# Optimization experiments

Measured on AMD Instinct MI355X. Metric: run time of the kernel, lower is better.

The kernel has to match this reference:

```python
import jax, jax.numpy as jnp
import numpy as np

INF = 1.0e12
V, EMB, H, H2 = 50000, 300, 512, 1024
EDGE, EEMB = 4, 32
B, TS, TQ = 16, 400, 33
MAX_OOV = 100
EXT = V + MAX_OOV
COV_HYPER = 1.0


def gru_cell(x, h, Wi, Wh, bi, bh):
    # torch GRU cell, gate order r,z,n
    gx = x @ Wi.T + bi
    gh = h @ Wh.T + bh
    hd = h.shape[-1]
    r = jax.nn.sigmoid(gx[:, :hd] + gh[:, :hd])
    z = jax.nn.sigmoid(gx[:, hd:2 * hd] + gh[:, hd:2 * hd])
    n = jnp.tanh(gx[:, 2 * hd:] + r * gh[:, 2 * hd:])
    return (1.0 - z) * n + z * h


def gru_scan(xs, h0, Wi, Wh, bi, bh, reverse=False):
    def step(h, x):
        hn = gru_cell(x, h, Wi, Wh, bi, bh)
        return hn, hn
    return jax.lax.scan(step, h0, xs, reverse=reverse)


def setup_inputs() -> dict:
    key = jax.random.key(0)
    ks = iter(jax.random.split(key, 64))
    def rp(*shape):
        return jax.random.normal(next(ks), shape, jnp.float32) * 0.05
    d = {}
    d['enc_emb'] = rp(V, EMB); d['ans_emb'] = rp(EDGE, EEMB); d['dec_emb'] = rp(V, EMB)
    in0 = EMB + EEMB
    d['eWi0'] = rp(2, 3 * H, in0); d['eWh0'] = rp(2, 3 * H, H); d['ebi0'] = rp(2, 3 * H); d['ebh0'] = rp(2, 3 * H)
    d['eWi1'] = rp(2, 3 * H, 2 * H); d['eWh1'] = rp(2, 3 * H, H); d['ebi1'] = rp(2, 3 * H); d['ebh1'] = rp(2, 3 * H)
    d['trans_W'] = rp(H2, H2); d['trans_b'] = rp(H2)
    d['upd_W'] = rp(H2, 2 * H2); d['gate_W'] = rp(H2, 2 * H2)
    din0 = EMB + H2
    d['dWi0'] = rp(3 * H2, din0); d['dWh0'] = rp(3 * H2, H2); d['dbi0'] = rp(3 * H2); d['dbh0'] = rp(3 * H2)
    d['dWi1'] = rp(3 * H2, H2); d['dWh1'] = rp(3 * H2, H2); d['dbi1'] = rp(3 * H2); d['dbh1'] = rp(3 * H2)
    d['dtrans_W'] = rp(H2, H2); d['dtrans_b'] = rp(H2)
    d['pW1'] = rp(H2, 2 * H2); d['pb1'] = rp(H2); d['pW2'] = rp(V, H2); d['pb2'] = rp(V)
    d['input_s'] = jax.random.randint(next(ks), (B, TS), 1, V)
    ext = jax.random.randint(next(ks), (B, TS), 0, EXT)
    d['ext_src_ids'] = ext.at[0, 0].set(EXT - 1)  # pin num_oov = MAX_OOV
    d['input_q'] = jax.random.randint(next(ks), (B, TQ), 1, V)
    d['input_a'] = jax.random.randint(next(ks), (B, TS), 0, EDGE)
    d['s_pos'] = jax.random.randint(next(ks), (B, TS), 0, TS)
    return d


def reference(enc_emb, ans_emb, dec_emb,
              eWi0, eWh0, ebi0, ebh0, eWi1, eWh1, ebi1, ebh1,
              trans_W, trans_b, upd_W, gate_W,
              dWi0, dWh0, dbi0, dbh0, dWi1, dWh1, dbi1, dbh1,
              dtrans_W, dtrans_b, pW1, pb1, pW2, pb2,
              input_s, ext_src_ids, input_q, input_a, s_pos):
    mask = jnp.sign(input_s)  # [B,TS] (all ones by construction)
    # ---------------- encoder ----------------
    emb = jnp.concatenate([enc_emb[input_s], ans_emb[input_a]], -1)  # [B,TS,EMB+EEMB]
    xs = emb.transpose(1, 0, 2)  # [TS,B,*]
    h0 = jnp.zeros((B, H), emb.dtype)
    h_list = []
    for (Wi, Wh, bi, bh) in ((eWi0, eWh0, ebi0, ebh0), (eWi1, eWh1, ebi1, ebh1)):
        hf, yf = gru_scan(xs, h0, Wi[0], Wh[0], bi[0], bh[0])
        hb, yb = gru_scan(xs, h0, Wi[1], Wh[1], bi[1], bh[1], reverse=True)
        xs = jnp.concatenate([yf, yb], -1)
        h_list.append(jnp.concatenate([hf, hb], -1))  # [B,H2]
    output = xs.transpose(1, 0, 2)  # [B,TS,H2]
    memories = output @ trans_W.T + trans_b
    # gated self-attention
    energies = jnp.einsum('btd,bsd->bts', output, memories)
    energies = jnp.where(mask[:, None, :] == 0, -INF, energies)
    scores = jax.nn.softmax(energies, -1)
    ctx = jnp.einsum('bts,bsd->btd', scores, output)
    inp = jnp.concatenate([output, ctx], -1)
    f_t = jnp.tanh(inp @ upd_W.T)
    g_t = jax.nn.sigmoid(inp @ gate_W.T)
    self_out = g_t * f_t + (1.0 - g_t) * output
    # answer-sentence attention (on memories, per original code)
    ans = jnp.where(input_a[..., None] == 0, 1.0, memories)
    e = memories * ans
    e = jnp.where(mask[..., None] == 0, -INF, e)
    e = jax.nn.softmax(e, axis=1)
    enc_out = self_out + e * memories
    # ---------------- decoder ----------------
    mem_d = enc_out @ dtrans_W.T + dtrans_b  # [B,TS,H2]
    emb_q = dec_emb[input_q[:, :-1]].transpose(1, 0, 2)  # [Tt,B,EMB]
    b_idx = jnp.arange(B)[:, None]

    def step(carry, emb_t):
        h0c, h1c, ctx_c, cov = carry
        rnn_in = jnp.concatenate([emb_t, ctx_c], -1)
        h0n = gru_cell(rnn_in, h0c, dWi0, dWh0, dbi0, dbh0)
        h1n = gru_cell(h0n, h1c, dWi1, dWh1, dbi1, dbh1)
        energy = jnp.einsum('bd,btd->bt', h1n, mem_d)
        sen_e = jnp.where(mask == 0, -INF, energy)
        cov_e = sen_e * (1.0 - cov)
        attn = jax.nn.softmax(cov_e, -1)
        new_ctx = jnp.einsum('bt,btd->bd', attn, mem_d)
        cov_loss = jnp.sum(jnp.minimum(attn, cov)) / B * COV_HYPER
        new_cov = cov + attn
        hid = jnp.tanh(jnp.concatenate([h1n, new_ctx], -1) @ pW1.T + pb1)
        logits = hid @ pW2.T + pb2
        ext = jnp.concatenate([logits, jnp.zeros((B, MAX_OOV), logits.dtype)], -1)
        out = jnp.full((B, EXT), -INF, logits.dtype).at[b_idx, ext_src_ids].max(cov_e)
        out = jnp.where(out == -INF, 0.0, out)
        lg = ext + out
        lg = jnp.where(lg == 0.0, -INF, lg)
        return (h0n, h1n, new_ctx, new_cov), (lg, cov_loss)

    init = (h_list[0], h_list[1], jnp.zeros((B, H2), emb.dtype), jnp.zeros((B, TS), emb.dtype))
    _, (lgs, covl) = jax.lax.scan(step, init, emb_q)
    return lgs.transpose(1, 0, 2), jnp.sum(covl) / lgs.shape[0]


if __name__ == '__main__':
    o = reference(**setup_inputs())
    print(o[0].shape, o[1])
```

## Files before the change

### kernel.cpp

```cpp
#include <hip/hip_runtime.h>
#include <stdint.h>

#define TSN 400
#define NB 16
#define HENC 512
#define HD2 1024
#define G3E 1536
#define G3D 3072
#define EMBD 300
#define AEMB 32
#define NV 50000
#define NEXT 50100
#define NVP 50176
#define NTT 32
#define NEG_INF (-1.0e12f)

typedef __attribute__((ext_vector_type(8))) short bf16x8;
typedef __attribute__((ext_vector_type(4))) float f32x4;

__device__ __forceinline__ ushort f2bf(float f) {
  unsigned u = __float_as_uint(f);
  unsigned r = (u + 0x7fffu + ((u >> 16) & 1u)) >> 16;
  return (ushort)r;
}
__device__ __forceinline__ float bf2f(ushort h) {
  return __uint_as_float((unsigned)h << 16);
}
__device__ __forceinline__ unsigned agat_ld(const unsigned* p) {
  return __hip_atomic_load(p, __ATOMIC_RELAXED, __HIP_MEMORY_SCOPE_AGENT);
}
__device__ __forceinline__ void agat_st(unsigned* p, unsigned v) {
  __hip_atomic_store(p, v, __ATOMIC_RELAXED, __HIP_MEMORY_SCOPE_AGENT);
}

__global__ __launch_bounds__(256) void k_embed_bf(
    const float* __restrict__ enc_emb, const float* __restrict__ ans_emb,
    const int* __restrict__ input_s, const int* __restrict__ input_a,
    ushort* __restrict__ X0)
{
  long i = (long)blockIdx.x*256 + threadIdx.x;
  if (i >= (long)TSN*NB*384) return;
  int c = (int)(i % 384);
  long r = i / 384;
  int b = (int)(r % NB);
  int t = (int)(r / NB);
  float v = 0.f;
  if (c < EMBD) v = enc_emb[(long)input_s[b*TSN + t]*EMBD + c];
  else if (c < 332) v = ans_emb[(long)input_a[b*TSN + t]*AEMB + (c - EMBD)];
  X0[i] = f2bf(v);
}

__global__ __launch_bounds__(256) void k_embq_bf(
    const float* __restrict__ dec_emb, const int* __restrict__ input_q,
    ushort* __restrict__ EQ)
{
  long i = (long)blockIdx.x*256 + threadIdx.x;
  if (i >= (long)NTT*NB*320) return;
  int c = (int)(i % 320);
  long r = i / 320;
  int b = (int)(r % NB);
  int s = (int)(r / NB);
  EQ[i] = (c < EMBD) ? f2bf(dec_emb[(long)input_q[b*33 + s]*EMBD + c]) : (ushort)0;
}

__global__ __launch_bounds__(256) void k_castw(
    const float* __restrict__ src, ushort* __restrict__ dst,
    int Nsrc, long total, int Ksrc, int Kdst, int ldsrc, int coloff)
{
  long i = (long)blockIdx.x*256 + threadIdx.x;
  if (i >= total) return;
  int k = (int)(i % Kdst);
  long n = i / Kdst;
  float v = (n < Nsrc && k < Ksrc) ? src[n*ldsrc + coloff + k] : 0.f;
  dst[i] = f2bf(v);
}

__global__ __launch_bounds__(256) void k_cast(
    const float* __restrict__ s, ushort* __restrict__ d, long n)
{
  long i = (long)blockIdx.x*256 + threadIdx.x;
  if (i >= n) return;
  d[i] = f2bf(s[i]);
}

__global__ __launch_bounds__(256) void k_transpose_hh(
    const ushort* __restrict__ in, ushort* __restrict__ out)
{
  __shared__ ushort tb[32][33];
  int b = blockIdx.z;
  int r0 = blockIdx.x*32, c0 = blockIdx.y*32;
  int tx = threadIdx.x & 31, ty = threadIdx.x >> 5;
  #pragma unroll
  for (int i = 0; i < 32; i += 8) {
    int r = r0 + ty + i, c = c0 + tx;
    tb[ty+i][tx] = (r < TSN) ? in[((long)b*TSN + r)*1024 + c] : (ushort)0;
  }
  __syncthreads();
  #pragma unroll
  for (int i = 0; i < 32; i += 8) {
    int c = c0 + ty + i, r = r0 + tx;
    out[((long)b*1024 + c)*448 + r] = tb[tx][ty+i];
  }
}

__global__ __launch_bounds__(256) void k_mfma_nt(
    const ushort* __restrict__ Ab, const ushort* __restrict__ Wb,
    const float* __restrict__ bias, float* __restrict__ Cb, ushort* __restrict__ C2b,
    int M, int N, int K, int lda, int ldw, int ldc,
    long sA, long sW, long sC, long sBias, int accum, int act)
{
  __shared__ ushort As[64][72];
  __shared__ ushort Ws[64][72];
  const ushort* A = Ab + (long)blockIdx.z * sA;
  const ushort* W = Wb + (long)blockIdx.z * sW;
  float* C = Cb ? Cb + (long)blockIdx.z * sC : nullptr;
  const float* bi = bias ? bias + (long)blockIdx.z * sBias : nullptr;
  const int m0 = blockIdx.x*64, n0 = blockIdx.y*64;
  const int tid = threadIdx.x;
  const int wave = tid >> 6, lane = tid & 63;
  const int wm = wave >> 1, wn = wave & 1;
  const int lr = lane & 15, kg = lane >> 4;
  f32x4 acc[2][2] = {};
  for (int k0 = 0; k0 < K; k0 += 64) {
    __syncthreads();
    #pragma unroll
    for (int it = 0; it < 2; ++it) {
      int sidx = tid + it*256;
      int r = sidx >> 3, c = (sidx & 7)*8;
      bf16x8 av = {};
      bf16x8 wv = {};
      if (m0 + r < M) av = *(const bf16x8*)&A[(long)(m0+r)*lda + k0 + c];
      if (n0 + r < N) wv = *(const bf16x8*)&W[(long)(n0+r)*ldw + k0 + c];
      *(bf16x8*)&As[r][c] = av;
      *(bf16x8*)&Ws[r][c] = wv;
    }
    __syncthreads();
    #pragma unroll
    for (int kk = 0; kk < 2; ++kk) {
      bf16x8 af[2], bf[2];
      #pragma unroll
      for (int mt = 0; mt < 2; ++mt)
        af[mt] = *(const bf16x8*)&As[wm*32 + mt*16 + lr][kk*32 + kg*8];
      #pragma unroll
      for (int nt = 0; nt < 2; ++nt)
        bf[nt] = *(const bf16x8*)&Ws[wn*32 + nt*16 + lr][kk*32 + kg*8];
      #pragma unroll
      for (int mt = 0; mt < 2; ++mt)
        #pragma unroll
        for (int nt = 0; nt < 2; ++nt)
          acc[mt][nt] = __builtin_amdgcn_mfma_f32_16x16x32_bf16(af[mt], bf[nt], acc[mt][nt], 0, 0, 0);
    }
  }
  #pragma unroll
  for (int mt = 0; mt < 2; ++mt) {
    #pragma unroll
    for (int r = 0; r < 4; ++r) {
      int m = m0 + wm*32 + mt*16 + kg*4 + r;
      if (m >= M) continue;
      #pragma unroll
      for (int nt = 0; nt < 2; ++nt) {
        int n = n0 + wn*32 + nt*16 + lr;
        if (n >= N) continue;
        float v = acc[mt][nt][r];
        if (accum && C) v += C[(long)m*ldc + n];
        if (bi)    v += bi[n];
        if (act == 1) v = tanhf(v);
        else if (act == 2) v = 1.f/(1.f + expf(-v));
        if (C) C[(long)m*ldc + n] = v;
        if (C2b) C2b[(long)blockIdx.z*sC + (long)m*ldc + n] = f2bf(v);
      }
    }
  }
}

__global__ __launch_bounds__(256, 1) void k_scan_mfma(
    const ushort* __restrict__ GXf, const ushort* __restrict__ GXb,
    const ushort* __restrict__ Whb,
    const float* __restrict__ bh,
    ushort* __restrict__ Ybf, int bmajor,
    float* __restrict__ hfin,
    ushort* __restrict__ hpp,
    int* __restrict__ slots)
{
  const int bid = blockIdx.x;
  const int tid = threadIdx.x;
  const int wg = bid*4 + (tid >> 6);
  const int lane = tid & 63;
  const int lr = lane & 15, kg = lane >> 4;
  const int dir = wg >> 5, jt = wg & 31;
  const int j = jt*16 + lr;
  __shared__ ushort hsm[16][520];
  const ushort* Wp0 = Whb + ((long)(dir*G3E + j)        << 9) + kg*8;
  const ushort* Wp1 = Whb + ((long)(dir*G3E + 512 + j)  << 9) + kg*8;
  const ushort* Wp2 = Whb + ((long)(dir*G3E + 1024 + j) << 9) + kg*8;
  bf16x8 W0[16], W1[16], W2[16];
  #pragma unroll
  for (int i = 0; i < 16; ++i) {
    W0[i] = *(const bf16x8*)(Wp0 + i*32);
    W1[i] = *(const bf16x8*)(Wp1 + i*32);
    W2[i] = *(const bf16x8*)(Wp2 + i*32);
  }
  const float bh0 = bh[dir*G3E + j];
  const float bh1 = bh[dir*G3E + 512 + j];
  const float bh2 = bh[dir*G3E + 1024 + j];
  const ushort* GX = dir ? GXb : GXf;
  unsigned* hppu = (unsigned*)hpp;
  int* myslot = slots + dir*256 + (bid & 7)*32;
  int* dslots = slots + dir*256;
  float hreg[4] = {0.f, 0.f, 0.f, 0.f};
  float g0[4], g1[4], g2[4];
  {
    const int t0 = dir ? (TSN - 1) : 0;
    const ushort* gxp = GX + (long)t0*NB*G3E + j;
    #pragma unroll
    for (int r = 0; r < 4; ++r) {
      const ushort* g = gxp + (long)(kg*4 + r)*G3E;
      g0[r] = bf2f(g[0]); g1[r] = bf2f(g[512]); g2[r] = bf2f(g[1024]);
    }
  }
  for (int s = 0; s < TSN; ++s) {
    const int cur = s & 1;
    {
      const unsigned* hin = hppu + (cur*2 + dir)*4096;
      unsigned vdw[16];
      #pragma unroll
      for (int i = 0; i < 16; ++i) vdw[i] = agat_ld(hin + i*256 + tid);
      #pragma unroll
      for (int i = 0; i < 16; ++i) {
        int idx = i*256 + tid;
        int b = idx >> 8, jd = idx & 255;
        *(unsigned*)&hsm[b][jd*2] = vdw[i];
      }
    }
    __syncthreads();
    f32x4 a0 = {}, a1 = {}, a2 = {};
    #pragma unroll
    for (int i = 0; i < 16; ++i) {
      bf16x8 hf = *(const bf16x8*)&hsm[lr][kg*8 + i*32];
      a0 = __builtin_amdgcn_mfma_f32_16x16x32_bf16(hf, W0[i], a0, 0, 0, 0);
      a1 = __builtin_amdgcn_mfma_f32_16x16x32_bf16(hf, W1[i], a1, 0, 0, 0);
      a2 = __builtin_amdgcn_mfma_f32_16x16x32_bf16(hf, W2[i], a2, 0, 0, 0);
    }
    const int t = dir ? (TSN - 1 - s) : s;
    const int obase = ((cur^1)*2 + dir)*16*512;
    float hsave[4];
    #pragma unroll
    for (int r = 0; r < 4; ++r) {
      int b = kg*4 + r;
      float rr = 1.f/(1.f + expf(-(g0[r] + a0[r] + bh0)));
      float zz = 1.f/(1.f + expf(-(g1[r] + a1[r] + bh1)));
      float nn = tanhf(g2[r] + rr*(a2[r] + bh2));
      float hn = (1.f - zz)*nn + zz*hreg[r];
      hreg[r] = hn;
      hsave[r] = hn;
      unsigned hv = f2bf(hn);
      unsigned pv = (unsigned)__shfl_xor((int)hv, 1);
      if ((lr & 1) == 0)
        agat_st(hppu + ((obase + b*512 + j) >> 1), hv | (pv << 16));
    }
    if (s + 1 < TSN) {
      asm volatile("s_waitcnt vmcnt(0)" ::: "memory");
      __syncthreads();
      if (tid == 0)
        agat_st((unsigned*)myslot, (unsigned)(s + 1));
      {
        const int tn = dir ? (TSN - 2 - s) : (s + 1);
        const ushort* gxp = GX + (long)tn*NB*G3E + j;
        #pragma unroll
        for (int r = 0; r < 4; ++r) {
          const ushort* g = gxp + (long)(kg*4 + r)*G3E;
          g0[r] = bf2f(g[0]); g1[r] = bf2f(g[512]); g2[r] = bf2f(g[1024]);
        }
      }
      #pragma unroll
      for (int r = 0; r < 4; ++r) {
        int b = kg*4 + r;
        long yi = bmajor ? ((long)b*TSN + t)*1024 + dir*512 + j
                         : ((long)t*NB + b)*1024 + dir*512 + j;
        Ybf[yi] = f2bf(hsave[r]);
      }
      if (tid < 8) {
        while ((int)agat_ld((const unsigned*)(dslots + tid*32)) < s + 1)
          __builtin_amdgcn_s_sleep(1);
      }
      __syncthreads();
    } else {
      #pragma unroll
      for (int r = 0; r < 4; ++r) {
        int b = kg*4 + r;
        long yi = bmajor ? ((long)b*TSN + t)*1024 + dir*512 + j
                         : ((long)t*NB + b)*1024 + dir*512 + j;
        Ybf[yi] = f2bf(hsave[r]);
        hfin[b*1024 + dir*512 + j] = hsave[r];
      }
    }
  }
}

__global__ __launch_bounds__(256) void k_softmax_bf(
    const float* __restrict__ E, ushort* __restrict__ S)
{
  long row = blockIdx.x;
  const float* x = E + row*TSN;
  ushort* o = S + row*448;
  int tid = threadIdx.x;
  float v0 = (tid < TSN) ? x[tid] : -INFINITY;
  float v1 = (tid + 256 < TSN) ? x[tid + 256] : -INFINITY;
  __shared__ float red[256];
  red[tid] = fmaxf(v0, v1); __syncthreads();
  for (int oo = 128; oo; oo >>= 1) { if (tid < oo) red[tid] = fmaxf(red[tid], red[tid+oo]); __syncthreads(); }
  float m = red[0]; __syncthreads();
  float e0 = (tid < TSN) ? expf(v0 - m) : 0.f;
  float e1 = (tid + 256 < TSN) ? expf(v1 - m) : 0.f;
  red[tid] = e0 + e1; __syncthreads();
  for (int oo = 128; oo; oo >>= 1) { if (tid < oo) red[tid] += red[tid+oo]; __syncthreads(); }
  float inv = 1.f/red[0];
  if (tid < 192) o[tid + 256] = (tid + 256 < TSN) ? f2bf(e1*inv) : (ushort)0;
  o[tid] = f2bf(e0*inv);
}

__global__ __launch_bounds__(256) void k_ansatt2(
    const ushort* __restrict__ memsb, const float* __restrict__ ft,
    const float* __restrict__ gt, const ushort* __restrict__ outpb,
    const int* __restrict__ input_a, ushort* __restrict__ encb)
{
  int b = blockIdx.x >> 2;
  int d = (blockIdx.x & 3)*256 + threadIdx.x;
  __shared__ int ia[TSN];
  for (int i = threadIdx.x; i < TSN; i += 256) ia[i] = input_a[b*TSN + i];
  __syncthreads();
  float m = -INFINITY;
  #pragma unroll 4
  for (int t = 0; t < TSN; ++t) {
    float v = bf2f(memsb[((long)b*TSN + t)*1024 + d]);
    float e = ia[t] ? v*v : v;
    m = fmaxf(m, e);
  }
  float ssum = 0.f;
  #pragma unroll 4
  for (int t = 0; t < TSN; ++t) {
    float v = bf2f(memsb[((long)b*TSN + t)*1024 + d]);
    float e = ia[t] ? v*v : v;
    ssum += expf(e - m);
  }
  float inv = 1.f/ssum;
  #pragma unroll 4
  for (int t = 0; t < TSN; ++t) {
    long idx = ((long)b*TSN + t)*1024 + d;
    float v = bf2f(memsb[idx]);
    float e = ia[t] ? v*v : v;
    float gg = gt[idx];
    float selfo = gg*ft[idx] + (1.f - gg)*bf2f(outpb[idx]);
    encb[idx] = f2bf(selfo + expf(e - m)*inv*v);
  }
}

__global__ __launch_bounds__(128) void k_gru_dec(
    const ushort* __restrict__ A1, const ushort* __restrict__ W1,
    const ushort* __restrict__ A2, const ushort* __restrict__ W2,
    const float* __restrict__ gxadd, const float* __restrict__ bi,
    const float* __restrict__ bh,
    const float* __restrict__ hprev, float* __restrict__ hout,
    ushort* __restrict__ houtb, ushort* __restrict__ catb)
{
  const int wv = threadIdx.x >> 6;
  const int lane = threadIdx.x & 63;
  const int lr = lane & 15, kg = lane >> 4;
  const int j = blockIdx.x*16 + lr;
  const int kb = wv*512;
  __shared__ float psum[6][16][16];
  const ushort* w1p0 = W1 + ((long)(j)        << 10) + kb + kg*8;
  const ushort* w1p1 = W1 + ((long)(1024 + j) << 10) + kb + kg*8;
  const ushort* w1p2 = W1 + ((long)(2048 + j) << 10) + kb + kg*8;
  const ushort* w2p0 = W2 + ((long)(j)        << 10) + kb + kg*8;
  const ushort* w2p1 = W2 + ((long)(1024 + j) << 10) + kb + kg*8;
  const ushort* w2p2 = W2 + ((long)(2048 + j) << 10) + kb + kg*8;
  const ushort* a1p = A1 + lr*1024 + kb + kg*8;
  const ushort* a2p = A2 + lr*1024 + kb + kg*8;
  f32x4 x0 = {}, x1 = {}, x2 = {}, h0 = {}, h1 = {}, h2 = {};
  #pragma unroll 4
  for (int k0 = 0; k0 < 512; k0 += 32) {
    bf16x8 a1v = *(const bf16x8*)(a1p + k0);
    bf16x8 a2v = *(const bf16x8*)(a2p + k0);
    x0 = __builtin_amdgcn_mfma_f32_16x16x32_bf16(a1v, *(const bf16x8*)(w1p0 + k0), x0, 0, 0, 0);
    x1 = __builtin_amdgcn_mfma_f32_16x16x32_bf16(a1v, *(const bf16x8*)(w1p1 + k0), x1, 0, 0, 0);
    x2 = __builtin_amdgcn_mfma_f32_16x16x32_bf16(a1v, *(const bf16x8*)(w1p2 + k0), x2, 0, 0, 0);
    h0 = __builtin_amdgcn_mfma_f32_16x16x32_bf16(a2v, *(const bf16x8*)(w2p0 + k0), h0, 0, 0, 0);
    h1 = __builtin_amdgcn_mfma_f32_16x16x32_bf16(a2v, *(const bf16x8*)(w2p1 + k0), h1, 0, 0, 0);
    h2 = __builtin_amdgcn_mfma_f32_16x16x32_bf16(a2v, *(const bf16x8*)(w2p2 + k0), h2, 0, 0, 0);
  }
  if (wv == 1) {
    #pragma unroll
    for (int r = 0; r < 4; ++r) {
      int b = kg*4 + r;
      psum[0][b][lr] = x0[r]; psum[1][b][lr] = x1[r]; psum[2][b][lr] = x2[r];
      psum[3][b][lr] = h0[r]; psum[4][b][lr] = h1[r]; psum[5][b][lr] = h2[r];
    }
  }
  __syncthreads();
  if (wv == 0) {
    float bi0 = bi ? bi[j] : 0.f, bi1 = bi ? bi[1024 + j] : 0.f, bi2 = bi ? bi[2048 + j] : 0.f;
    float bh0 = bh[j], bh1 = bh[1024 + j], bh2 = bh[2048 + j];
    #pragma unroll
    for (int r = 0; r < 4; ++r) {
      int b = kg*4 + r;
      float gxa0 = gxadd ? gxadd[(long)b*G3D + j]        : 0.f;
      float gxa1 = gxadd ? gxadd[(long)b*G3D + 1024 + j] : 0.f;
      float gxa2 = gxadd ? gxadd[(long)b*G3D + 2048 + j] : 0.f;
      float gx0 = x0[r] + psum[0][b][lr] + gxa0 + bi0;
      float gx1 = x1[r] + psum[1][b][lr] + gxa1 + bi1;
      float gx2 = x2[r] + psum[2][b][lr] + gxa2 + bi2;
      float gh0 = h0[r] + psum[3][b][lr] + bh0;
      float gh1 = h1[r] + psum[4][b][lr] + bh1;
      float gh2 = h2[r] + psum[5][b][lr] + bh2;
      float rr = 1.f/(1.f + expf(-(gx0 + gh0)));
      float zz = 1.f/(1.f + expf(-(gx1 + gh1)));
      float nn = tanhf(gx2 + rr*gh2);
      float hp = hprev[b*1024 + j];
      float hn = (1.f - zz)*nn + zz*hp;
      hout[b*1024 + j] = hn;
      houtb[b*1024 + j] = f2bf(hn);
      if (catb) catb[(long)b*2048 + j] = f2bf(hn);
    }
  }
}

__global__ __launch_bounds__(1024) void k_dec_attn2(
    const ushort* __restrict__ h1b, const ushort* __restrict__ memdb,
    float* __restrict__ cov, float* __restrict__ covOut, float* __restrict__ covacc,
    ushort* __restrict__ ctxn, ushort* __restrict__ catb)
{
  const int b = blockIdx.x, tid = threadIdx.x;
  const int wv = tid >> 6, ln = tid & 63;
  __shared__ float sc[TSN];
  __shared__ float at[TSN];
  __shared__ float red[1024];
  float hreg[16];
  {
    bf16x8 hv0 = *(const bf16x8*)&h1b[b*1024 + ln*16];
    bf16x8 hv1 = *(const bf16x8*)&h1b[b*1024 + ln*16 + 8];
    #pragma unroll
    for (int e = 0; e < 8; ++e) { hreg[e] = bf2f((ushort)hv0[e]); hreg[8+e] = bf2f((ushort)hv1[e]); }
  }
  for (int t = wv; t < TSN; t += 16) {
    const ushort* row = memdb + ((long)b*TSN + t)*1024 + ln*16;
    bf16x8 r0 = *(const bf16x8*)row;
    bf16x8 r1 = *(const bf16x8*)(row + 8);
    float p = 0.f;
    #pragma unroll
    for (int e = 0; e < 8; ++e) p += hreg[e]*bf2f((ushort)r0[e]) + hreg[8+e]*bf2f((ushort)r1[e]);
    #pragma unroll
    for (int off = 32; off; off >>= 1) p += __shfl_xor(p, off);
    if (ln == 0) sc[t] = p;
  }
  __syncthreads();
  float ce = -INFINITY, co = 0.f;
  if (tid < TSN) { co = cov[b*TSN + tid]; ce = sc[tid]*(1.f - co); }
  red[tid] = ce; __syncthreads();
  for (int o = 512; o; o >>= 1) { if (tid < o) red[tid] = fmaxf(red[tid], red[tid+o]); __syncthreads(); }
  float m = red[0]; __syncthreads();
  float ex = (tid < TSN) ? expf(ce - m) : 0.f;
  red[tid] = ex; __syncthreads();
  for (int o = 512; o; o >>= 1) { if (tid < o) red[tid] += red[tid+o]; __syncthreads(); }
  float inv = 1.f/red[0]; __syncthreads();
  float closs = 0.f;
  if (tid < TSN) {
    float a = ex*inv;
    at[tid] = a;
    cov[b*TSN + tid] = co + a;
    covOut[b*TSN + tid] = ce;
    closs = fminf(a, co);
  }
  red[tid] = closs; __syncthreads();
  for (int o = 512; o; o >>= 1) { if (tid < o) red[tid] += red[tid+o]; __syncthreads(); }
  if (tid == 0) atomicAdd(covacc, red[0]);
  __syncthreads();
  float s = 0.f;
  const ushort* col = memdb + (long)b*TSN*1024 + tid;
  #pragma unroll 8
  for (int t = 0; t < TSN; ++t) s += at[t]*bf2f(col[(long)t*1024]);
  ushort hv = f2bf(s);
  ctxn[b*1024 + tid] = hv;
  catb[(long)b*2048 + 1024 + tid] = hv;
}

__global__ __launch_bounds__(128) void k_hid(
    const ushort* __restrict__ catb, const ushort* __restrict__ W,
    const float* __restrict__ pb1, ushort* __restrict__ hidb)
{
  const int wv = threadIdx.x >> 6;
  const int lane = threadIdx.x & 63;
  const int lr = lane & 15, kg = lane >> 4;
  const int n = blockIdx.x*16 + lr;
  const int kb = wv*1024;
  __shared__ float ps[16][16];
  f32x4 acc = {};
  const ushort* ap = catb + lr*2048 + kb + kg*8;
  const ushort* wp = W + ((long)n << 11) + kb + kg*8;
  #pragma unroll 8
  for (int k0 = 0; k0 < 1024; k0 += 32)
    acc = __builtin_amdgcn_mfma_f32_16x16x32_bf16(*(const bf16x8*)(ap + k0), *(const bf16x8*)(wp + k0), acc, 0, 0, 0);
  if (wv == 1) {
    #pragma unroll
    for (int r = 0; r < 4; ++r) ps[kg*4 + r][lr] = acc[r];
  }
  __syncthreads();
  if (wv == 0) {
    float bv = pb1[n];
    #pragma unroll
    for (int r = 0; r < 4; ++r) {
      int b = kg*4 + r;
      hidb[b*1024 + n] = f2bf(tanhf(acc[r] + ps[b][lr] + bv));
    }
  }
}

__global__ __launch_bounds__(256) void k_logits_all(
    const ushort* __restrict__ hidAll,
    const ushort* __restrict__ pW2b,
    const float* __restrict__ pb2,
    float* __restrict__ outp)
{
  const int wave = threadIdx.x >> 6, lane = threadIdx.x & 63;
  const int lr = lane & 15, kg = lane >> 4;
  const int n0 = blockIdx.x*256 + wave*64;
  const int m0 = blockIdx.y*128;
  f32x4 acc[8][4] = {};
  for (int k0 = 0; k0 < 1024; k0 += 32) {
    bf16x8 bfr[4];
    #pragma unroll
    for (int nt = 0; nt < 4; ++nt)
      bfr[nt] = *(const bf16x8*)&pW2b[(long)(n0 + nt*16 + lr)*1024 + k0 + kg*8];
    #pragma unroll
    for (int mt = 0; mt < 8; ++mt) {
      bf16x8 af = *(const bf16x8*)&hidAll[(long)(m0 + mt*16 + lr)*1024 + k0 + kg*8];
      #pragma unroll
      for (int nt = 0; nt < 4; ++nt)
        acc[mt][nt] = __builtin_amdgcn_mfma_f32_16x16x32_bf16(af, bfr[nt], acc[mt][nt], 0, 0, 0);
    }
  }
  #pragma unroll
  for (int nt = 0; nt < 4; ++nt) {
    int v = n0 + nt*16 + lr;
    if (v >= NEXT) continue;
    float pb = (v < NV) ? pb2[v] : 0.f;
    #pragma unroll
    for (int mt = 0; mt < 8; ++mt) {
      #pragma unroll
      for (int r = 0; r < 4; ++r) {
        int m = m0 + mt*16 + kg*4 + r;
        int s = m >> 4, b = m & 15;
        float e = (v < NV) ? (acc[mt][nt][r] + pb) : 0.f;
        if (e == 0.f) e = NEG_INF;
        outp[((long)b*NTT + s)*NEXT + v] = e;
      }
    }
  }
}

__device__ __forceinline__ float dec_f(unsigned e) {
  return (e & 0x80000000u) ? __uint_as_float(e ^ 0x80000000u) : __uint_as_float(~e);
}
__global__ __launch_bounds__(512) void k_compose_all(
    const int* __restrict__ ids, const float* __restrict__ coveAll,
    unsigned* __restrict__ ubuf, float* __restrict__ outp)
{
  int b = blockIdx.x, tid = threadIdx.x;
  int v = 0;
  if (tid < TSN) v = ids[b*TSN + tid];
  unsigned* up = ubuf + (long)b*NEXT;
  for (int s = 0; s < NTT; ++s) {
    if (tid < TSN) {
      float ce = coveAll[((long)s*NB + b)*TSN + tid];
      unsigned bb = __float_as_uint(ce);
      unsigned enc = (bb & 0x80000000u) ? ~bb : (bb | 0x80000000u);
      atomicMax(&up[v], enc);
    }
    __syncthreads();
    if (tid < TSN) {
      unsigned u = __hip_atomic_load(&up[v], __ATOMIC_RELAXED, __HIP_MEMORY_SCOPE_AGENT);
      float o = dec_f(u);
      long oi = ((long)b*NTT + s)*NEXT + v;
      float e = outp[oi];
      if (e == NEG_INF) e = 0.f;
      float lg = e + o;
      if (lg == 0.f) lg = NEG_INF;
      outp[oi] = lg;
    }
    __syncthreads();
    if (tid < TSN)
      __hip_atomic_store(&up[v], 0u, __ATOMIC_RELAXED, __HIP_MEMORY_SCOPE_AGENT);
    __syncthreads();
  }
}

__global__ void k_covout(const float* __restrict__ covacc, float* __restrict__ outp)
{
  outp[(long)NB*NTT*NEXT] = covacc[0] * (1.0f/(NB*NTT));
}

extern "C" void kernel_launch(void* const* d_in, const int* in_sizes, int n_in,
                              void* d_out, int out_size, void* d_ws, size_t ws_size,
                              hipStream_t stream) {
  (void)in_sizes; (void)n_in; (void)out_size; (void)ws_size;
  const float* enc_emb = (const float*)d_in[0];
  const float* ans_emb = (const float*)d_in[1];
  const float* dec_emb = (const float*)d_in[2];
  const float* eWi0 = (const float*)d_in[3];
  const float* eWh0 = (const float*)d_in[4];
  const float* ebi0 = (const float*)d_in[5];
  const float* ebh0 = (const float*)d_in[6];
  const float* eWi1 = (const float*)d_in[7];
  const float* eWh1 = (const float*)d_in[8];
  const float* ebi1 = (const float*)d_in[9];
  const float* ebh1 = (const float*)d_in[10];
  const float* trans_W = (const float*)d_in[11];
  const float* trans_b = (const float*)d_in[12];
  const float* upd_W = (const float*)d_in[13];
  const float* gate_W = (const float*)d_in[14];
  const float* dWi0 = (const float*)d_in[15];
  const float* dWh0 = (const float*)d_in[16];
  const float* dbi0 = (const float*)d_in[17];
  const float* dbh0 = (const float*)d_in[18];
  const float* dWi1 = (const float*)d_in[19];
  const float* dWh1 = (const float*)d_in[20];
  const float* dbi1 = (const float*)d_in[21];
  const float* dbh1 = (const float*)d_in[22];
  const float* dtrans_W = (const float*)d_in[23];
  const float* dtrans_b = (const float*)d_in[24];
  const float* pW1 = (const float*)d_in[25];
  const float* pb1 = (const float*)d_in[26];
  const float* pW2 = (const float*)d_in[27];
  const float* pb2 = (const float*)d_in[28];
  const int* input_s = (const int*)d_in[29];
  const int* ext_ids = (const int*)d_in[30];
  const int* input_q = (const int*)d_in[31];
  const int* input_a = (const int*)d_in[32];
  float* out = (float*)d_out;

  float* ws = (float*)d_ws;
  size_t off = 0;
  auto alloc = [&](size_t n) { float* p = ws + off; off += (n + 15) & ~(size_t)15; return p; };
  auto alloch = [&](size_t nh) { return (ushort*)alloc((nh + 1) / 2); };

  ushort* hpp  = alloch(2ull*2*NB*HENC);
  int*   bar   = (int*)alloc(2048);
  float* covacc= alloc(4);
  float* cov   = alloc(NB*TSN);
  unsigned* ubuf = (unsigned*)alloc((size_t)NB*NEXT);
  float* hfin0 = alloc(NB*HD2);
  float* hfin1 = alloc(NB*HD2);
  float* dh0   = alloc(2ull*NB*HD2);
  float* dh1   = alloc(2ull*NB*HD2);
  ushort* h0b  = alloch(2ull*NB*HD2);
  ushort* h1b  = alloch(2ull*NB*HD2);
  ushort* ctxbf= alloch(2ull*NB*HD2);
  ushort* catbf= alloch((size_t)NB*2048);
  ushort* hidAll = alloch((size_t)NTT*NB*HD2);
  float* coveAll = alloc((size_t)NTT*NB*TSN);

  ushort* eWi0c   = alloch(2ull*G3E*384);
  ushort* eWi1c   = alloch(2ull*G3E*1024);
  ushort* Whb0    = alloch(2ull*G3E*HENC);
  ushort* Whb1    = alloch(2ull*G3E*HENC);
  ushort* transWb = alloch(1024ull*1024);
  ushort* updWb   = alloch(1024ull*2048);
  ushort* gateWb  = alloch(1024ull*2048);
  ushort* dtransWb= alloch(1024ull*1024);
  ushort* dWi0e   = alloch(3072ull*320);
  ushort* dWi0c   = alloch(3072ull*1024);
  ushort* dWh0b   = alloch(3072ull*1024);
  ushort* dWi1b   = alloch(3072ull*1024);
  ushort* dWh1b   = alloch(3072ull*1024);
  ushort* pW1b    = alloch(1024ull*2048);

  size_t regionStart = off;
  float*  GXr  = alloc(2ull*6400*G3E);
  ushort* GXbf = (ushort*)GXr;
  ushort* X0c  = alloch(6400ull*384);
  ushort* Y0bf = alloch(6400ull*1024);
  float*  ft   = alloc(6400ull*HD2);
  ushort* pW2b   = (ushort*)(ws + regionStart);
  ushort* outpTb = (ushort*)(ws + regionStart + 26000000);

  ushort* outpbf = alloch(6400ull*HD2);
  ushort* memsbf = alloch(6400ull*HD2);
  float*  scratchC = alloc(6400ull*HD2);
  float*  energ  = alloc((size_t)NB*TSN*TSN);
  ushort* scoresb= alloch((size_t)NB*TSN*448);
  ushort* ctx_bf = alloch(6400ull*HD2);
  ushort* memd_bf= alloch(6400ull*HD2);
  ushort* encbf  = alloch(6400ull*HD2);
  ushort* embqb  = alloch(512ull*320);
  float*  embGX  = alloc(512ull*G3D);

  k_embed_bf<<<9600, 256, 0, stream>>>(enc_emb, ans_emb, input_s, input_a, X0c);
  k_castw<<<4608, 256, 0, stream>>>(eWi0, eWi0c, 3072, 3072ull*384, 332, 384, 332, 0);
  k_castw<<<12288, 256, 0, stream>>>(eWi1, eWi1c, 3072, 3072ull*1024, 1024, 1024, 1024, 0);
  k_castw<<<6144, 256, 0, stream>>>(eWh0, Whb0, 3072, 3072ull*512, 512, 512, 512, 0);
  k_castw<<<6144, 256, 0, stream>>>(eWh1, Whb1, 3072, 3072ull*512, 512, 512, 512, 0);
  k_castw<<<4096, 256, 0, stream>>>(trans_W, transWb, 1024, 1024ull*1024, 1024, 1024, 1024, 0);
  k_castw<<<8192, 256, 0, stream>>>(upd_W,  updWb,  1024, 1024ull*2048, 2048, 2048, 2048, 0);
  k_castw<<<8192, 256, 0, stream>>>(gate_W, gateWb, 1024, 1024ull*2048, 2048, 2048, 2048, 0);
  k_castw<<<4096, 256, 0, stream>>>(dtrans_W, dtransWb, 1024, 1024ull*1024, 1024, 1024, 1024, 0);
  k_castw<<<3840, 256, 0, stream>>>(dWi0, dWi0e, 3072, 3072ull*320, 300, 320, 1324, 0);
  k_castw<<<12288, 256, 0, stream>>>(dWi0, dWi0c, 3072, 3072ull*1024, 1024, 1024, 1324, 300);
  k_castw<<<12288, 256, 0, stream>>>(dWh0, dWh0b, 3072, 3072ull*1024, 1024, 1024, 1024, 0);
  k_castw<<<12288, 256, 0, stream>>>(dWi1, dWi1b, 3072, 3072ull*1024, 1024, 1024, 1024, 0);
  k_castw<<<12288, 256, 0, stream>>>(dWh1, dWh1b, 3072, 3072ull*1024, 1024, 1024, 1024, 0);
  k_castw<<<8192, 256, 0, stream>>>(pW1, pW1b, 1024, 1024ull*2048, 2048, 2048, 2048, 0);

  hipMemsetAsync(bar, 0, 8192, stream);

  k_mfma_nt<<<dim3(100,24,2), 256, 0, stream>>>(X0c, eWi0c, ebi0, nullptr, GXbf,
      6400, G3E, 384, 384, 384, G3E, 0, (long)G3E*384, 6400ull*G3E, G3E, 0, 0);
  hipMemsetAsync(hpp, 0, 2ull*2*NB*HENC*2, stream);
  k_scan_mfma<<<16, 256, 0, stream>>>(GXbf, GXbf + 6400ull*G3E, Whb0, ebh0,
      Y0bf, 0, hfin0, hpp, bar);
  k_mfma_nt<<<dim3(100,24,2), 256, 0, stream>>>(Y0bf, eWi1c, ebi1, nullptr, GXbf,
      6400, G3E, 1024, 1024, 1024, G3E, 0, (long)G3E*1024, 6400ull*G3E, G3E, 0, 0);
  hipMemsetAsync(hpp, 0, 2ull*2*NB*HENC*2, stream);
  k_scan_mfma<<<16, 256, 0, stream>>>(GXbf, GXbf + 6400ull*G3E, Whb1, ebh1,
      outpbf, 1, hfin1, hpp, bar + 512);

  k_mfma_nt<<<dim3(100,16,1), 256, 0, stream>>>(outpbf, transWb, trans_b, scratchC, memsbf,
      6400, HD2, 1024, 1024, 1024, HD2, 0, 0, 0, 0, 0, 0);
  k_mfma_nt<<<dim3(7,7,16), 256, 0, stream>>>(outpbf, memsbf, nullptr, energ, nullptr,
      TSN, TSN, 1024, 1024, 1024, TSN, (long)TSN*1024, (long)TSN*1024, (long)TSN*TSN, 0, 0, 0);
  k_softmax_bf<<<NB*TSN, 256, 0, stream>>>(energ, scoresb);
  k_transpose_hh<<<dim3(14,32,16), 256, 0, stream>>>(outpbf, outpTb);
  k_mfma_nt<<<dim3(7,16,16), 256, 0, stream>>>(scoresb, outpTb, nullptr, scratchC, ctx_bf,
      TSN, HD2, 448, 448, 448, HD2, (long)TSN*448, (long)HD2*448, (long)TSN*HD2, 0, 0, 0);
  k_mfma_nt<<<dim3(100,16,1), 256, 0, stream>>>(outpbf, updWb,        nullptr, ft, nullptr,
      6400, HD2, 1024, 1024, 2048, HD2, 0, 0, 0, 0, 0, 0);
  k_mfma_nt<<<dim3(100,16,1), 256, 0, stream>>>(ctx_bf, updWb + 1024, nullptr, ft, nullptr,
      6400, HD2, 1024, 1024, 2048, HD2, 0, 0, 0, 0, 1, 1);
  k_mfma_nt<<<dim3(100,16,1), 256, 0, stream>>>(outpbf, gateWb,       nullptr, scratchC, nullptr,
      6400, HD2, 1024, 1024, 2048, HD2, 0, 0, 0, 0, 0, 0);
  k_mfma_nt<<<dim3(100,16,1), 256, 0, stream>>>(ctx_bf, gateWb + 1024, nullptr, scratchC, nullptr,
      6400, HD2, 1024, 1024, 2048, HD2, 0, 0, 0, 0, 1, 2);
  k_ansatt2<<<64, 256, 0, stream>>>(memsbf, ft, scratchC, outpbf, input_a, encbf);
  k_castw<<<200704, 256, 0, stream>>>(pW2, pW2b, NV, (long)NVP*1024, 1024, 1024, 1024, 0);
  k_mfma_nt<<<dim3(100,16,1), 256, 0, stream>>>(encbf, dtransWb, dtrans_b, scratchC, memd_bf,
      6400, HD2, 1024, 1024, 1024, HD2, 0, 0, 0, 0, 0, 0);

  k_embq_bf<<<640, 256, 0, stream>>>(dec_emb, input_q, embqb);
  k_mfma_nt<<<dim3(8,48,1), 256, 0, stream>>>(embqb, dWi0e, dbi0, embGX, nullptr,
      NTT*NB, G3D, 320, 320, 320, G3D, 0, 0, 0, 0, 0, 0);

  hipMemsetAsync(cov, 0, (size_t)NB*TSN*4, stream);
  hipMemsetAsync(covacc, 0, 4, stream);
  hipMemsetAsync(ubuf, 0, (size_t)NB*NEXT*4, stream);
  hipMemsetAsync(ctxbf, 0, (size_t)NB*HD2*2, stream);
  hipMemcpyAsync(dh0, hfin0, (size_t)NB*HD2*4, hipMemcpyDeviceToDevice, stream);
  hipMemcpyAsync(dh1, hfin1, (size_t)NB*HD2*4, hipMemcpyDeviceToDevice, stream);
  k_cast<<<64, 256, 0, stream>>>(hfin0, h0b, 16384);
  k_cast<<<64, 256, 0, stream>>>(hfin1, h1b, 16384);

  for (int s = 0; s < NTT; ++s) {
    int cur = s & 1, nxt = cur ^ 1;
    float* h0c = dh0 + (size_t)cur*NB*HD2;  float* h0n = dh0 + (size_t)nxt*NB*HD2;
    float* h1c = dh1 + (size_t)cur*NB*HD2;  float* h1n = dh1 + (size_t)nxt*NB*HD2;
    ushort* h0bc = h0b + (size_t)cur*NB*HD2; ushort* h0bn = h0b + (size_t)nxt*NB*HD2;
    ushort* h1bc = h1b + (size_t)cur*NB*HD2; ushort* h1bn = h1b + (size_t)nxt*NB*HD2;
    ushort* ctxc = ctxbf + (size_t)cur*NB*HD2; ushort* ctxn = ctxbf + (size_t)nxt*NB*HD2;

    k_gru_dec<<<64, 128, 0, stream>>>(ctxc, dWi0c, h0bc, dWh0b,
        embGX + (size_t)s*NB*G3D, nullptr, dbh0, h0c, h0n, h0bn, nullptr);
    k_gru_dec<<<64, 128, 0, stream>>>(h0bn, dWi1b, h1bc, dWh1b,
        nullptr, dbi1, dbh1, h1c, h1n, h1bn, catbf);
    k_dec_attn2<<<NB, 1024, 0, stream>>>(h1bn, memd_bf,
        cov, coveAll + (size_t)s*NB*TSN, covacc, ctxn, catbf);
    k_hid<<<64, 128, 0, stream>>>(catbf, pW1b, pb1, hidAll + (size_t)s*NB*HD2);
  }
  k_logits_all<<<dim3(196, 4), 256, 0, stream>>>(hidAll, pW2b, pb2, out);
  k_compose_all<<<NB, 512, 0, stream>>>(ext_ids, coveAll, ubuf, out);
  k_covout<<<1, 1, 0, stream>>>(covacc, out);
}
```

Measured before the change: 6.138 ms.

## Fuse update/gate GEMMs into one concatenated GEMM and split decoder attention across blocks

The four update/gate GEMMs (self and context halves of upd_W and gate_W) become one 6400x2048x2048 GEMM. Its input is a concatenated [outp|ctx] bf16 buffer and its output is bf16, with tanh and sigmoid moved into k_ansatt2. This cuts kernel launches, removes the fp32 intermediate traffic and the split-K accumulation passes. The per-step decoder attention now runs on 64 blocks of 256 threads instead of 16 blocks of 1024. Partial scores are exchanged through global memory behind a spin-wait grid barrier, which raises parallelism but adds barrier overhead and relies on all 64 blocks being co-resident. The bf16 intermediates add rounding error.

```diff
diff --git a/kernel.cpp b/kernel.cpp
--- a/kernel.cpp
+++ b/kernel.cpp
@@ -81,6 +81,16 @@
   long i = (long)blockIdx.x*256 + threadIdx.x;
   if (i >= n) return;
   d[i] = f2bf(s[i]);
+}
+
+__global__ __launch_bounds__(256) void k_catcopy(
+    const unsigned* __restrict__ src, unsigned* __restrict__ dst)
+{
+  long i = (long)blockIdx.x*256 + threadIdx.x;
+  if (i >= 6400l*512) return;
+  long r = i >> 9;
+  int c = (int)(i & 511);
+  dst[(r << 10) + c] = src[i];
 }
 
 __global__ __launch_bounds__(256) void k_transpose_hh(
@@ -320,8 +330,8 @@
 }
 
 __global__ __launch_bounds__(256) void k_ansatt2(
-    const ushort* __restrict__ memsb, const float* __restrict__ ft,
-    const float* __restrict__ gt, const ushort* __restrict__ outpb,
+    const ushort* __restrict__ memsb, const ushort* __restrict__ ftgt,
+    const ushort* __restrict__ outpb,
     const int* __restrict__ input_a, ushort* __restrict__ encb)
 {
   int b = blockIdx.x >> 2;
@@ -347,10 +357,13 @@
   #pragma unroll 4
   for (int t = 0; t < TSN; ++t) {
     long idx = ((long)b*TSN + t)*1024 + d;
+    long idx2 = ((long)b*TSN + t)*2048 + d;
     float v = bf2f(memsb[idx]);
     float e = ia[t] ? v*v : v;
-    float gg = gt[idx];
-    float selfo = gg*ft[idx] + (1.f - gg)*bf2f(outpb[idx]);
+    float fraw = bf2f(ftgt[idx2]);
+    float graw = bf2f(ftgt[idx2 + 1024]);
+    float gg = 1.f/(1.f + expf(-graw));
+    float selfo = gg*tanhf(fraw) + (1.f - gg)*bf2f(outpb[idx]);
     encb[idx] = f2bf(selfo + expf(e - m)*inv*v);
   }
 }
@@ -425,63 +438,106 @@
   }
 }
 
-__global__ __launch_bounds__(1024) void k_dec_attn2(
+__global__ __launch_bounds__(256) void k_dec_attn3(
     const ushort* __restrict__ h1b, const ushort* __restrict__ memdb,
-    float* __restrict__ cov, float* __restrict__ covOut, float* __restrict__ covacc,
-    ushort* __restrict__ ctxn, ushort* __restrict__ catb)
-{
-  const int b = blockIdx.x, tid = threadIdx.x;
-  const int wv = tid >> 6, ln = tid & 63;
-  __shared__ float sc[TSN];
+    float* __restrict__ cov, float* __restrict__ coveS, float* __restrict__ covacc,
+    float* __restrict__ scb,
+    ushort* __restrict__ ctxn, ushort* __restrict__ catb,
+    int* __restrict__ slots, int epoch)
+{
+  const int bid = blockIdx.x, tid = threadIdx.x;
+  const int b = bid >> 2, q = bid & 3;
+  const int wv = tid >> 6, lane = tid & 63;
   __shared__ float at[TSN];
-  __shared__ float red[1024];
-  float hreg[16];
+  __shared__ float red[256];
+  __shared__ float psD[4][64][4];
+  float hr[16];
   {
-    bf16x8 hv0 = *(const bf16x8*)&h1b[b*1024 + ln*16];
-    bf16x8 hv1 = *(const bf16x8*)&h1b[b*1024 + ln*16 + 8];
-    #pragma unroll
-    for (int e = 0; e < 8; ++e) { hreg[e] = bf2f((ushort)hv0[e]); hreg[8+e] = bf2f((ushort)hv1[e]); }
-  }
-  for (int t = wv; t < TSN; t += 16) {
-    const ushort* row = memdb + ((long)b*TSN + t)*1024 + ln*16;
+    bf16x8 hv0 = *(const bf16x8*)&h1b[b*1024 + lane*16];
+    bf16x8 hv1 = *(const bf16x8*)&h1b[b*1024 + lane*16 + 8];
+    #pragma unroll
+    for (int e = 0; e < 8; ++e) { hr[e] = bf2f((ushort)hv0[e]); hr[8+e] = bf2f((ushort)hv1[e]); }
+  }
+  #pragma unroll 2
+  for (int i = 0; i < 25; ++i) {
+    int t = q*100 + wv*25 + i;
+    const ushort* row = memdb + ((long)b*TSN + t)*1024 + lane*16;
     bf16x8 r0 = *(const bf16x8*)row;
     bf16x8 r1 = *(const bf16x8*)(row + 8);
     float p = 0.f;
     #pragma unroll
-    for (int e = 0; e < 8; ++e) p += hreg[e]*bf2f((ushort)r0[e]) + hreg[8+e]*bf2f((ushort)r1[e]);
+    for (int e = 0; e < 8; ++e) p += hr[e]*bf2f((ushort)r0[e]) + hr[8+e]*bf2f((ushort)r1[e]);
     #pragma unroll
     for (int off = 32; off; off >>= 1) p += __shfl_xor(p, off);
-    if (ln == 0) sc[t] = p;
-  }
+    if (lane == 0) agat_st((unsigned*)&scb[b*TSN + t], __float_as_uint(p));
+  }
+  asm volatile("s_waitcnt vmcnt(0)" ::: "memory");
   __syncthreads();
-  float ce = -INFINITY, co = 0.f;
-  if (tid < TSN) { co = cov[b*TSN + tid]; ce = sc[tid]*(1.f - co); }
-  red[tid] = ce; __syncthreads();
-  for (int o = 512; o; o >>= 1) { if (tid < o) red[tid] = fmaxf(red[tid], red[tid+o]); __syncthreads(); }
-  float m = red[0]; __syncthreads();
-  float ex = (tid < TSN) ? expf(ce - m) : 0.f;
-  red[tid] = ex; __syncthreads();
-  for (int o = 512; o; o >>= 1) { if (tid < o) red[tid] += red[tid+o]; __syncthreads(); }
-  float inv = 1.f/red[0]; __syncthreads();
-  float closs = 0.f;
-  if (tid < TSN) {
-    float a = ex*inv;
-    at[tid] = a;
-    cov[b*TSN + tid] = co + a;
-    covOut[b*TSN + tid] = ce;
-    closs = fminf(a, co);
-  }
-  red[tid] = closs; __syncthreads();
-  for (int o = 512; o; o >>= 1) { if (tid < o) red[tid] += red[tid+o]; __syncthreads(); }
-  if (tid == 0) atomicAdd(covacc, red[0]);
+  if (tid == 0) agat_st((unsigned*)(slots + bid*32), (unsigned)epoch);
+  if (tid < 64) {
+    while ((int)agat_ld((const unsigned*)(slots + tid*32)) < epoch)
+      __builtin_amdgcn_s_sleep(1);
+  }
   __syncthreads();
-  float s = 0.f;
-  const ushort* col = memdb + (long)b*TSN*1024 + tid;
-  #pragma unroll 8
-  for (int t = 0; t < TSN; ++t) s += at[t]*bf2f(col[(long)t*1024]);
-  ushort hv = f2bf(s);
-  ctxn[b*1024 + tid] = hv;
-  catb[(long)b*2048 + 1024 + tid] = hv;
+  {
+    bool t1v = tid < 144;
+    float sc0 = __uint_as_float(agat_ld((const unsigned*)&scb[b*TSN + tid]));
+    float sc1 = t1v ? __uint_as_float(agat_ld((const unsigned*)&scb[b*TSN + 256 + tid])) : 0.f;
+    float co0 = cov[b*TSN + tid];
+    float co1 = t1v ? cov[b*TSN + 256 + tid] : 0.f;
+    float ce0 = sc0*(1.f - co0);
+    float ce1 = t1v ? sc1*(1.f - co1) : -INFINITY;
+    red[tid] = fmaxf(ce0, ce1); __syncthreads();
+    for (int o = 128; o; o >>= 1) { if (tid < o) red[tid] = fmaxf(red[tid], red[tid+o]); __syncthreads(); }
+    float m = red[0]; __syncthreads();
+    float ex0 = expf(ce0 - m), ex1 = t1v ? expf(ce1 - m) : 0.f;
+    red[tid] = ex0 + ex1; __syncthreads();
+    for (int o = 128; o; o >>= 1) { if (tid < o) red[tid] += red[tid+o]; __syncthreads(); }
+    float inv = 1.f/red[0]; __syncthreads();
+    float a0 = ex0*inv, a1 = ex1*inv;
+    at[tid] = a0;
+    if (t1v) at[256 + tid] = a1;
+    if (q == 0) {
+      coveS[b*TSN + tid] = ce0;
+      if (t1v) coveS[b*TSN + 256 + tid] = ce1;
+      cov[b*TSN + tid] = co0 + a0;
+      if (t1v) cov[b*TSN + 256 + tid] = co1 + a1;
+      red[tid] = fminf(a0, co0) + (t1v ? fminf(a1, co1) : 0.f);
+      __syncthreads();
+      for (int o = 128; o; o >>= 1) { if (tid < o) red[tid] += red[tid+o]; __syncthreads(); }
+      if (tid == 0) atomicAdd(covacc, red[0]);
+    }
+  }
+  __syncthreads();
+  {
+    float acc4[4] = {};
+    const int d0 = q*256 + lane*4;
+    const unsigned* base = (const unsigned*)memdb + (((long)b*TSN*1024 + d0) >> 1);
+    for (int t = wv*100; t < wv*100 + 100; ++t) {
+      float a = at[t];
+      const unsigned* p = base + (long)t*512;
+      unsigned dv0 = p[0], dv1 = p[1];
+      acc4[0] += a*bf2f((ushort)(dv0 & 0xffffu));
+      acc4[1] += a*bf2f((ushort)(dv0 >> 16));
+      acc4[2] += a*bf2f((ushort)(dv1 & 0xffffu));
+      acc4[3] += a*bf2f((ushort)(dv1 >> 16));
+    }
+    #pragma unroll
+    for (int e = 0; e < 4; ++e) psD[wv][lane][e] = acc4[e];
+    __syncthreads();
+    if (wv == 0) {
+      float c[4];
+      #pragma unroll
+      for (int e = 0; e < 4; ++e)
+        c[e] = psD[0][lane][e] + psD[1][lane][e] + psD[2][lane][e] + psD[3][lane][e];
+      unsigned w0 = (unsigned)f2bf(c[0]) | ((unsigned)f2bf(c[1]) << 16);
+      unsigned w1 = (unsigned)f2bf(c[2]) | ((unsigned)f2bf(c[3]) << 16);
+      unsigned* cp = (unsigned*)ctxn + ((b*1024 + d0) >> 1);
+      cp[0] = w0; cp[1] = w1;
+      unsigned* kp = (unsigned*)catb + (((long)b*2048 + 1024 + d0) >> 1);
+      kp[0] = w0; kp[1] = w1;
+    }
+  }
 }
 
 __global__ __launch_bounds__(128) void k_hid(
@@ -644,9 +700,10 @@
   auto alloch = [&](size_t nh) { return (ushort*)alloc((nh + 1) / 2); };
 
   ushort* hpp  = alloch(2ull*2*NB*HENC);
-  int*   bar   = (int*)alloc(2048);
+  int*   bar   = (int*)alloc(4096);
   float* covacc= alloc(4);
   float* cov   = alloc(NB*TSN);
+  float* scb   = alloc(NB*TSN);
   unsigned* ubuf = (unsigned*)alloc((size_t)NB*NEXT);
   float* hfin0 = alloc(NB*HD2);
   float* hfin1 = alloc(NB*HD2);
@@ -664,8 +721,7 @@
   ushort* Whb0    = alloch(2ull*G3E*HENC);
   ushort* Whb1    = alloch(2ull*G3E*HENC);
   ushort* transWb = alloch(1024ull*1024);
-  ushort* updWb   = alloch(1024ull*2048);
-  ushort* gateWb  = alloch(1024ull*2048);
+  ushort* fgWb    = alloch(2048ull*2048);
   ushort* dtransWb= alloch(1024ull*1024);
   ushort* dWi0e   = alloch(3072ull*320);
   ushort* dWi0c   = alloch(3072ull*1024);
@@ -679,16 +735,16 @@
   ushort* GXbf = (ushort*)GXr;
   ushort* X0c  = alloch(6400ull*384);
   ushort* Y0bf = alloch(6400ull*1024);
-  float*  ft   = alloc(6400ull*HD2);
-  ushort* pW2b   = (ushort*)(ws + regionStart);
-  ushort* outpTb = (ushort*)(ws + regionStart + 26000000);
+  alloc(6400ull*HD2);
+  ushort* ftgt_bf = (ushort*)(ws + regionStart);
+  ushort* pW2b    = (ushort*)(ws + regionStart);
+  ushort* outpTb  = (ushort*)(ws + regionStart + 26000000);
 
   ushort* outpbf = alloch(6400ull*HD2);
   ushort* memsbf = alloch(6400ull*HD2);
-  float*  scratchC = alloc(6400ull*HD2);
+  ushort* catE   = alloch(6400ull*2048);
   float*  energ  = alloc((size_t)NB*TSN*TSN);
   ushort* scoresb= alloch((size_t)NB*TSN*448);
-  ushort* ctx_bf = alloch(6400ull*HD2);
   ushort* memd_bf= alloch(6400ull*HD2);
   ushort* encbf  = alloch(6400ull*HD2);
   ushort* embqb  = alloch(512ull*320);
@@ -700,8 +756,8 @@
   k_castw<<<6144, 256, 0, stream>>>(eWh0, Whb0, 3072, 3072ull*512, 512, 512, 512, 0);
   k_castw<<<6144, 256, 0, stream>>>(eWh1, Whb1, 3072, 3072ull*512, 512, 512, 512, 0);
   k_castw<<<4096, 256, 0, stream>>>(trans_W, transWb, 1024, 1024ull*1024, 1024, 1024, 1024, 0);
-  k_castw<<<8192, 256, 0, stream>>>(upd_W,  updWb,  1024, 1024ull*2048, 2048, 2048, 2048, 0);
-  k_castw<<<8192, 256, 0, stream>>>(gate_W, gateWb, 1024, 1024ull*2048, 2048, 2048, 2048, 0);
+  k_castw<<<8192, 256, 0, stream>>>(upd_W,  fgWb,              1024, 1024ull*2048, 2048, 2048, 2048, 0);
+  k_castw<<<8192, 256, 0, stream>>>(gate_W, fgWb + 1024ull*2048, 1024, 1024ull*2048, 2048, 2048, 2048, 0);
   k_castw<<<4096, 256, 0, stream>>>(dtrans_W, dtransWb, 1024, 1024ull*1024, 1024, 1024, 1024, 0);
   k_castw<<<3840, 256, 0, stream>>>(dWi0, dWi0e, 3072, 3072ull*320, 300, 320, 1324, 0);
   k_castw<<<12288, 256, 0, stream>>>(dWi0, dWi0c, 3072, 3072ull*1024, 1024, 1024, 1324, 300);
@@ -710,7 +766,7 @@
   k_castw<<<12288, 256, 0, stream>>>(dWh1, dWh1b, 3072, 3072ull*1024, 1024, 1024, 1024, 0);
   k_castw<<<8192, 256, 0, stream>>>(pW1, pW1b, 1024, 1024ull*2048, 2048, 2048, 2048, 0);
 
-  hipMemsetAsync(bar, 0, 8192, stream);
+  hipMemsetAsync(bar, 0, 16384, stream);
 
   k_mfma_nt<<<dim3(100,24,2), 256, 0, stream>>>(X0c, eWi0c, ebi0, nullptr, GXbf,
       6400, G3E, 384, 384, 384, G3E, 0, (long)G3E*384, 6400ull*G3E, G3E, 0, 0);
@@ -723,25 +779,20 @@
   k_scan_mfma<<<16, 256, 0, stream>>>(GXbf, GXbf + 6400ull*G3E, Whb1, ebh1,
       outpbf, 1, hfin1, hpp, bar + 512);
 
-  k_mfma_nt<<<dim3(100,16,1), 256, 0, stream>>>(outpbf, transWb, trans_b, scratchC, memsbf,
+  k_mfma_nt<<<dim3(100,16,1), 256, 0, stream>>>(outpbf, transWb, trans_b, nullptr, memsbf,
       6400, HD2, 1024, 1024, 1024, HD2, 0, 0, 0, 0, 0, 0);
   k_mfma_nt<<<dim3(7,7,16), 256, 0, stream>>>(outpbf, memsbf, nullptr, energ, nullptr,
       TSN, TSN, 1024, 1024, 1024, TSN, (long)TSN*1024, (long)TSN*1024, (long)TSN*TSN, 0, 0, 0);
   k_softmax_bf<<<NB*TSN, 256, 0, stream>>>(energ, scoresb);
   k_transpose_hh<<<dim3(14,32,16), 256, 0, stream>>>(outpbf, outpTb);
-  k_mfma_nt<<<dim3(7,16,16), 256, 0, stream>>>(scoresb, outpTb, nullptr, scratchC, ctx_bf,
-      TSN, HD2, 448, 448, 448, HD2, (long)TSN*448, (long)HD2*448, (long)TSN*HD2, 0, 0, 0);
-  k_mfma_nt<<<dim3(100,16,1), 256, 0, stream>>>(outpbf, updWb,        nullptr, ft, nullptr,
-      6400, HD2, 1024, 1024, 2048, HD2, 0, 0, 0, 0, 0, 0);
-  k_mfma_nt<<<dim3(100,16,1), 256, 0, stream>>>(ctx_bf, updWb + 1024, nullptr, ft, nullptr,
-      6400, HD2, 1024, 1024, 2048, HD2, 0, 0, 0, 0, 1, 1);
-  k_mfma_nt<<<dim3(100,16,1), 256, 0, stream>>>(outpbf, gateWb,       nullptr, scratchC, nullptr,
-      6400, HD2, 1024, 1024, 2048, HD2, 0, 0, 0, 0, 0, 0);
-  k_mfma_nt<<<dim3(100,16,1), 256, 0, stream>>>(ctx_bf, gateWb + 1024, nullptr, scratchC, nullptr,
-      6400, HD2, 1024, 1024, 2048, HD2, 0, 0, 0, 0, 1, 2);
-  k_ansatt2<<<64, 256, 0, stream>>>(memsbf, ft, scratchC, outpbf, input_a, encbf);
+  k_mfma_nt<<<dim3(7,16,16), 256, 0, stream>>>(scoresb, outpTb, nullptr, nullptr, catE + 1024,
+      TSN, HD2, 448, 448, 448, 2048, (long)TSN*448, (long)HD2*448, (long)TSN*2048, 0, 0, 0);
+  k_catcopy<<<12800, 256, 0, stream>>>((const unsigned*)outpbf, (unsigned*)catE);
+  k_mfma_nt<<<dim3(100,32,1), 256, 0, stream>>>(catE, fgWb, nullptr, nullptr, ftgt_bf,
+      6400, 2048, 2048, 2048, 2048, 2048, 0, 0, 0, 0, 0, 0);
+  k_ansatt2<<<64, 256, 0, stream>>>(memsbf, ftgt_bf, outpbf, input_a, encbf);
   k_castw<<<200704, 256, 0, stream>>>(pW2, pW2b, NV, (long)NVP*1024, 1024, 1024, 1024, 0);
-  k_mfma_nt<<<dim3(100,16,1), 256, 0, stream>>>(encbf, dtransWb, dtrans_b, scratchC, memd_bf,
+  k_mfma_nt<<<dim3(100,16,1), 256, 0, stream>>>(encbf, dtransWb, dtrans_b, nullptr, memd_bf,
       6400, HD2, 1024, 1024, 1024, HD2, 0, 0, 0, 0, 0, 0);
 
   k_embq_bf<<<640, 256, 0, stream>>>(dec_emb, input_q, embqb);
@@ -769,8 +820,9 @@
         embGX + (size_t)s*NB*G3D, nullptr, dbh0, h0c, h0n, h0bn, nullptr);
     k_gru_dec<<<64, 128, 0, stream>>>(h0bn, dWi1b, h1bc, dWh1b,
         nullptr, dbi1, dbh1, h1c, h1n, h1bn, catbf);
-    k_dec_attn2<<<NB, 1024, 0, stream>>>(h1bn, memd_bf,
-        cov, coveAll + (size_t)s*NB*TSN, covacc, ctxn, catbf);
+    k_dec_attn3<<<64, 256, 0, stream>>>(h1bn, memd_bf,
+        cov, coveAll + (size_t)s*NB*TSN, covacc, scb, ctxn, catbf,
+        bar + 1024, s + 1);
     k_hid<<<64, 128, 0, stream>>>(catbf, pW1b, pb1, hidAll + (size_t)s*NB*HD2);
   }
   k_logits_all<<<dim3(196, 4), 256, 0, stream>>>(hidAll, pW2b, pb2, out);
```

Measured after the change: 6.001 ms. 2.2% less time.
